# Performance work log

Hardware: AMD Instinct MI355X
Metric: run time of the kernel (lower is better)

## Reference

```python
import jax, jax.numpy as jnp
import numpy as np

Z = 10        # number of negative samples per item
LAMB = 0.01   # L2 regularization weight


def setup_inputs() -> dict:
    key = jax.random.key(0)
    k = jax.random.split(key, 7)
    WE, DE, V, D, B, NG = 300, 256, 50000, 100000, 4096, 10
    return {
        "rv": jax.random.normal(k[0], (WE, V), dtype=jnp.float32),      # word embedding table (frozen in original)
        "rd": jax.random.normal(k[1], (DE, D), dtype=jnp.float32),      # document embedding table
        "proj": jax.random.normal(k[2], (DE, WE), dtype=jnp.float32) * (1.0 / np.sqrt(WE)),
        "beta": jax.random.uniform(k[3], (DE,), dtype=jnp.float32),
        "word_ids": jax.random.randint(k[4], (B, NG), 0, V),
        "doc_ids": jax.random.randint(k[5], (B,), 0, D),
        "neg_ids": jax.random.randint(k[6], (B, Z), 0, D),
    }


def reference(rv, rd, proj, beta, word_ids, doc_ids, neg_ids):
    # g: mean of n-gram word embeddings per sample -> (we, B)
    g = rv[:, word_ids].mean(axis=2)
    # norm: per-sample L2 normalization
    normed = g / jnp.linalg.norm(g, axis=0, keepdims=True)
    # f: project into document space -> (de, B)
    t_pre = proj @ normed
    # standardize across the batch (torch .std is unbiased, ddof=1);
    # NOTE: original divides by sqrt(std), faithfully reproduced
    mean = t_pre.mean(axis=1, keepdims=True)
    std = jnp.std(t_pre, axis=1, ddof=1, keepdims=True)
    t = jnp.clip((t_pre - mean) / jnp.sqrt(std) + beta[:, None], -1.0, 1.0)  # hardtanh
    # positive documents: (de, B)
    doc_emb = rd[:, doc_ids]
    p_pos = jnp.clip(jax.nn.sigmoid(jnp.sum(t * doc_emb, axis=0)), -0.999, 0.999)
    log_p = Z * jnp.log(p_pos)  # (B,)
    # negative samples: (de, B, Z)
    neg_emb = rd[:, neg_ids]
    p_neg = jnp.clip(jax.nn.sigmoid(jnp.einsum('db,dbz->bz', t, neg_emb)), -0.999, 0.999)
    nsample_log = jnp.sum(jnp.log(jnp.clip(1.0 - p_neg, 0.01, None)), axis=1)  # (B,)
    log_p_wave = (Z + 1) / (2 * Z) * (log_p + nsample_log)
    B = log_p_wave.shape[0]
    loss = jnp.sum(log_p_wave) / B + LAMB / (2 * B) * (jnp.sum(rd * rd) + jnp.sum(proj * proj))
    return loss
```

## Files before the change

kernel.cpp:

```cpp
#include <hip/hip_runtime.h>
#include <math.h>

#define WE 300
#define DEp 256
#define VV 50000
#define DDim 100000
#define BB 4096
#define NGc 10
#define RVT_STRIDE 304

__device__ __forceinline__ float wave_reduce(float v) {
    #pragma unroll
    for (int o = 32; o > 0; o >>= 1) v += __shfl_down(v, o, 64);
    return v;
}

__device__ __forceinline__ float wave_allreduce(float v) {
    #pragma unroll
    for (int o = 32; o > 0; o >>= 1) v += __shfl_xor(v, o, 64);
    return v;
}

__device__ __forceinline__ float logsigf(float x) {
    return (x >= 0.f) ? -log1pf(expf(-x)) : x - log1pf(expf(x));
}

__global__ void k_init(double* p, int n) {
    int i = blockIdx.x * blockDim.x + threadIdx.x;
    if (i < n) p[i] = 0.0;
}

__global__ __launch_bounds__(256) void k_trd(const float* __restrict__ in,
                                             float* __restrict__ out,
                                             double* __restrict__ reg_acc) {
    __shared__ float4 tile[32 * 64];
    const int N = DDim;
    int n0 = blockIdx.x * 32;
    int t = threadIdx.x;
    float ss = 0.f;
    #pragma unroll
    for (int i = 0; i < 2; ++i) {
        int flat = i * 256 + t;
        int qn = flat & 7;
        int qm = flat >> 3;
        int n = n0 + qn * 4;
        const float* p = in + (size_t)(qm * 4) * N + n;
        float4 v0 = *(const float4*)(p);
        float4 v1 = *(const float4*)(p + N);
        float4 v2 = *(const float4*)(p + 2 * (size_t)N);
        float4 v3 = *(const float4*)(p + 3 * (size_t)N);
        ss += v0.x * v0.x + v0.y * v0.y + v0.z * v0.z + v0.w * v0.w;
        ss += v1.x * v1.x + v1.y * v1.y + v1.z * v1.z + v1.w * v1.w;
        ss += v2.x * v2.x + v2.y * v2.y + v2.z * v2.z + v2.w * v2.w;
        ss += v3.x * v3.x + v3.y * v3.y + v3.z * v3.z + v3.w * v3.w;
        int r0 = qn * 4;
        tile[(r0 + 0) * 64 + (qm ^ (r0 + 0))] = make_float4(v0.x, v1.x, v2.x, v3.x);
        tile[(r0 + 1) * 64 + (qm ^ (r0 + 1))] = make_float4(v0.y, v1.y, v2.y, v3.y);
        tile[(r0 + 2) * 64 + (qm ^ (r0 + 2))] = make_float4(v0.z, v1.z, v2.z, v3.z);
        tile[(r0 + 3) * 64 + (qm ^ (r0 + 3))] = make_float4(v0.w, v1.w, v2.w, v3.w);
    }
    __syncthreads();
    size_t base = (size_t)n0 * DEp;
    #pragma unroll
    for (int i = 0; i < 8; ++i) {
        int j = i * 256 + t;
        int nl = j >> 6;
        int m4 = j & 63;
        *(float4*)(out + base + (size_t)j * 4) = tile[nl * 64 + (m4 ^ nl)];
    }
    float r = wave_reduce(ss);
    __shared__ float part[4];
    int lane = t & 63, wv = t >> 6;
    if (lane == 0) part[wv] = r;
    __syncthreads();
    if (t == 0)
        atomicAdd(reg_acc, (double)(part[0] + part[1] + part[2] + part[3]));
}

__global__ __launch_bounds__(256) void k_trv(const float* __restrict__ in,
                                             float* __restrict__ out) {
    __shared__ float4 tile[32 * 80];
    const int N = VV;
    int n0 = blockIdx.x * 32;
    int t = threadIdx.x;
    #pragma unroll
    for (int i = 0; i < 3; ++i) {
        int flat = i * 256 + t;
        if (flat < 600) {
            int qn = flat & 7;
            int qm = flat >> 3;
            int n = n0 + qn * 4;
            float4 v0, v1, v2, v3;
            if (n < N) {
                const float* p = in + (size_t)(qm * 4) * N + n;
                v0 = *(const float4*)(p);
                v1 = *(const float4*)(p + N);
                v2 = *(const float4*)(p + 2 * (size_t)N);
                v3 = *(const float4*)(p + 3 * (size_t)N);
            } else {
                v0 = v1 = v2 = v3 = make_float4(0.f, 0.f, 0.f, 0.f);
            }
            int r0 = qn * 4;
            tile[(r0 + 0) * 80 + (qm ^ ((r0 + 0) & 7))] = make_float4(v0.x, v1.x, v2.x, v3.x);
            tile[(r0 + 1) * 80 + (qm ^ ((r0 + 1) & 7))] = make_float4(v0.y, v1.y, v2.y, v3.y);
            tile[(r0 + 2) * 80 + (qm ^ ((r0 + 2) & 7))] = make_float4(v0.z, v1.z, v2.z, v3.z);
            tile[(r0 + 3) * 80 + (qm ^ ((r0 + 3) & 7))] = make_float4(v0.w, v1.w, v2.w, v3.w);
        }
    }
    __syncthreads();
    size_t base = (size_t)n0 * (RVT_STRIDE / 4);
    float4* out4 = (float4*)out;
    for (int i = 0; i < 10; ++i) {
        int j = i * 256 + t;
        if (j < 2432) {
            int nl = j / 76;
            int m4 = j - nl * 76;
            if (n0 + nl < N)
                out4[base + j] = tile[nl * 80 + (m4 ^ (nl & 7))];
        }
    }
}


__global__ __launch_bounds__(256) void k_gather2(const float* __restrict__ rvT,
                                                 const int* __restrict__ wid,
                                                 float* __restrict__ normed) {
    int wv = threadIdx.x >> 6, lane = threadIdx.x & 63;
    int b = blockIdx.x * 4 + wv;
    int id = 0;
    if (lane < NGc) id = wid[b * NGc + lane];
    float4 a  = make_float4(0.f, 0.f, 0.f, 0.f);
    float4 a2 = make_float4(0.f, 0.f, 0.f, 0.f);
    #pragma unroll
    for (int ng = 0; ng < NGc; ++ng) {
        int rid = __shfl(id, ng, 64);
        const float* row = rvT + (size_t)rid * RVT_STRIDE;
        float4 v = *(const float4*)(row + lane * 4);
        a.x += v.x; a.y += v.y; a.z += v.z; a.w += v.w;
        if (lane < 11) {
            float4 w = *(const float4*)(row + 256 + lane * 4);
            a2.x += w.x; a2.y += w.y; a2.z += w.z; a2.w += w.w;
        }
    }
    a.x *= 0.1f; a.y *= 0.1f; a.z *= 0.1f; a.w *= 0.1f;
    a2.x *= 0.1f; a2.y *= 0.1f; a2.z *= 0.1f; a2.w *= 0.1f;
    float ss = a.x * a.x + a.y * a.y + a.z * a.z + a.w * a.w
             + a2.x * a2.x + a2.y * a2.y + a2.z * a2.z + a2.w * a2.w;
    float s = wave_allreduce(ss);
    float s_inv = 1.0f / sqrtf(s);
    float* orow = normed + (size_t)b * WE;
    *(float4*)(orow + lane * 4) =
        make_float4(a.x * s_inv, a.y * s_inv, a.z * s_inv, a.w * s_inv);
    if (lane < 11)
        *(float4*)(orow + 256 + lane * 4) =
            make_float4(a2.x * s_inv, a2.y * s_inv, a2.z * s_inv, a2.w * s_inv);
}

__global__ __launch_bounds__(256) void k_loss2(const float* __restrict__ tpre,
                                               const float* __restrict__ meanf,
                                               const float* __restrict__ scalef,
                                               const float* __restrict__ beta,
                                               const float* __restrict__ rdT,
                                               const int* __restrict__ doc_ids,
                                               const int* __restrict__ neg_ids,
                                               double* __restrict__ acc) {
    int wv = threadIdx.x >> 6, lane = threadIdx.x & 63;
    int b = blockIdx.x * 4 + wv;

    float4 t4  = *(const float4*)(tpre + (size_t)b * DEp + lane * 4);
    float4 m4  = *(const float4*)(meanf + lane * 4);
    float4 sc4 = *(const float4*)(scalef + lane * 4);
    float4 be4 = *(const float4*)(beta + lane * 4);
    float tv0 = fminf(1.f, fmaxf(-1.f, (t4.x - m4.x) * sc4.x + be4.x));
    float tv1 = fminf(1.f, fmaxf(-1.f, (t4.y - m4.y) * sc4.y + be4.y));
    float tv2 = fminf(1.f, fmaxf(-1.f, (t4.z - m4.z) * sc4.z + be4.z));
    float tv3 = fminf(1.f, fmaxf(-1.f, (t4.w - m4.w) * sc4.w + be4.w));

    int id = 0;
    if (lane == 0) id = doc_ids[b];
    else if (lane < 11) id = neg_ids[b * NGc + lane - 1];

    float xv = 0.f;
    #pragma unroll
    for (int j = 0; j < 11; ++j) {
        int rid = __shfl(id, j, 64);
        float4 r4 = *(const float4*)(rdT + (size_t)rid * DEp + lane * 4);
        float p = tv0 * r4.x + tv1 * r4.y + tv2 * r4.z + tv3 * r4.w;
        p = wave_allreduce(p);
        if (lane == j) xv = p;
    }
    float contrib = 0.f;
    if (lane == 0)      contrib = 10.f * fminf(logsigf(xv), -1.0005003e-3f);
    else if (lane < 11) contrib = fmaxf(logsigf(-xv), -4.6051702f);
    #pragma unroll
    for (int o = 8; o > 0; o >>= 1) contrib += __shfl_down(contrib, o, 16);

    __shared__ float bp[4];
    if (lane == 0) bp[wv] = contrib;
    __syncthreads();
    if (threadIdx.x == 0)
        atomicAdd(acc, (double)(0.55f * (bp[0] + bp[1] + bp[2] + bp[3])));
}


__global__ __launch_bounds__(320) void k_gather(const float* __restrict__ rv,
                                                const int* __restrict__ wid,
                                                float* __restrict__ normed) {
    int b = blockIdx.x;
    int tid = threadIdx.x;
    __shared__ int ids[NGc];
    __shared__ float wpart[5];
    __shared__ float s_inv;
    if (tid < NGc) ids[tid] = wid[b * NGc + tid];
    __syncthreads();
    float g = 0.f;
    if (tid < WE) {
        const float* row = rv + (size_t)tid * VV;
        #pragma unroll
        for (int ng = 0; ng < NGc; ++ng) g += row[ids[ng]];
        g *= 0.1f;
    }
    float r = wave_reduce(g * g);
    int lane = tid & 63, wv = tid >> 6;
    if (lane == 0) wpart[wv] = r;
    __syncthreads();
    if (tid == 0) {
        float s = wpart[0] + wpart[1] + wpart[2] + wpart[3] + wpart[4];
        s_inv = 1.0f / sqrtf(s);
    }
    __syncthreads();
    if (tid < WE) normed[(size_t)b * WE + tid] = g * s_inv;
}

__global__ __launch_bounds__(256) void k_loss(const float* __restrict__ tpre,
                                              const float* __restrict__ meanf,
                                              const float* __restrict__ scalef,
                                              const float* __restrict__ beta,
                                              const float* __restrict__ rd,
                                              const int* __restrict__ doc_ids,
                                              const int* __restrict__ neg_ids,
                                              double* __restrict__ acc) {
    int b = blockIdx.x;
    int de = threadIdx.x;
    float t = tpre[(size_t)b * DEp + de];
    float tv = (t - meanf[de]) * scalef[de] + beta[de];
    tv = fminf(1.f, fmaxf(-1.f, tv));
    const float* rdrow = rd + (size_t)de * DDim;
    __shared__ int ids[11];
    if (de == 0) ids[0] = doc_ids[b];
    if (de >= 1 && de < 11) ids[de] = neg_ids[b * NGc + de - 1];
    __syncthreads();
    float prod[11];
    #pragma unroll
    for (int j = 0; j < 11; ++j) prod[j] = tv * rdrow[ids[j]];
    __shared__ float part[11][4];
    int lane = de & 63, wv = de >> 6;
    #pragma unroll
    for (int j = 0; j < 11; ++j) {
        float r = wave_reduce(prod[j]);
        if (lane == 0) part[j][wv] = r;
    }
    __syncthreads();
    if (de == 0) {
        float x0 = part[0][0] + part[0][1] + part[0][2] + part[0][3];
        float total = 10.f * fminf(logsigf(x0), -1.0005003e-3f);
        #pragma unroll
        for (int j = 1; j < 11; ++j) {
            float xj = part[j][0] + part[j][1] + part[j][2] + part[j][3];
            total += fmaxf(logsigf(-xj), -4.6051702f);
        }
        atomicAdd(acc, (double)(0.55f * total));
    }
}


__global__ __launch_bounds__(256) void k_gemm(const float* __restrict__ proj,
                                              const float* __restrict__ normed,
                                              float* __restrict__ tpre) {
    __shared__ float As[64 * 33];
    __shared__ float Bs[64 * 33];
    int tid = threadIdx.x;
    int tx = tid & 15, ty = tid >> 4;
    int de0 = blockIdx.y * 64;
    int b0  = blockIdx.x * 64;
    float acc[4][4] = {};
    int f = tid & 7, r0 = tid >> 3;
    for (int kt = 0; kt < 10; ++kt) {
        int k0 = kt * 32;
        __syncthreads();
        for (int rr = r0; rr < 64; rr += 32) {
            int k = k0 + f * 4;
            float4 va = make_float4(0.f, 0.f, 0.f, 0.f);
            float4 vb = make_float4(0.f, 0.f, 0.f, 0.f);
            if (k + 3 < WE) {
                va = *(const float4*)(proj + (size_t)(de0 + rr) * WE + k);
                vb = *(const float4*)(normed + (size_t)(b0 + rr) * WE + k);
            }
            float* ap = &As[rr * 33 + f * 4];
            ap[0] = va.x; ap[1] = va.y; ap[2] = va.z; ap[3] = va.w;
            float* bp = &Bs[rr * 33 + f * 4];
            bp[0] = vb.x; bp[1] = vb.y; bp[2] = vb.z; bp[3] = vb.w;
        }
        __syncthreads();
        #pragma unroll
        for (int k = 0; k < 32; ++k) {
            float a[4], bv[4];
            #pragma unroll
            for (int i = 0; i < 4; ++i) a[i] = As[(tx * 4 + i) * 33 + k];
            #pragma unroll
            for (int j = 0; j < 4; ++j) bv[j] = Bs[(ty * 4 + j) * 33 + k];
            #pragma unroll
            for (int j = 0; j < 4; ++j)
                #pragma unroll
                for (int i = 0; i < 4; ++i) acc[j][i] += a[i] * bv[j];
        }
    }
    #pragma unroll
    for (int jb = 0; jb < 4; ++jb) {
        int b = b0 + ty * 4 + jb;
        float4 v = make_float4(acc[jb][0], acc[jb][1], acc[jb][2], acc[jb][3]);
        *(float4*)(tpre + (size_t)b * DEp + de0 + tx * 4) = v;
    }
}

__global__ __launch_bounds__(256) void k_stats1(const float* __restrict__ tpre,
                                                double* __restrict__ rowsum,
                                                double* __restrict__ rowsq) {
    int de = threadIdx.x;
    int c0 = blockIdx.x * 64;
    float s = 0.f, ss = 0.f;
    for (int i = 0; i < 64; ++i) {
        float v = tpre[(size_t)(c0 + i) * DEp + de];
        s += v; ss += v * v;
    }
    atomicAdd(&rowsum[de], (double)s);
    atomicAdd(&rowsq[de], (double)ss);
}

__global__ void k_stats2(const double* __restrict__ rowsum, const double* __restrict__ rowsq,
                         float* __restrict__ meanf, float* __restrict__ scalef) {
    int de = threadIdx.x;
    double s = rowsum[de], ss = rowsq[de];
    double mean = s / (double)BB;
    double var = (ss - s * s / (double)BB) / (double)(BB - 1);
    double stdv = sqrt(var);
    meanf[de]  = (float)mean;
    scalef[de] = (float)(1.0 / sqrt(stdv));
}

__global__ __launch_bounds__(256) void k_reg(const float4* __restrict__ p, int n4,
                                             double* __restrict__ acc) {
    int idx = blockIdx.x * blockDim.x + threadIdx.x;
    int stride = gridDim.x * blockDim.x;
    float s = 0.f;
    for (int i = idx; i < n4; i += stride) {
        float4 v = p[i];
        s += v.x * v.x + v.y * v.y + v.z * v.z + v.w * v.w;
    }
    float r = wave_reduce(s);
    __shared__ float part[4];
    int lane = threadIdx.x & 63, wv = threadIdx.x >> 6;
    if (lane == 0) part[wv] = r;
    __syncthreads();
    if (threadIdx.x == 0)
        atomicAdd(acc, (double)(part[0] + part[1] + part[2] + part[3]));
}

__global__ void k_final(const double* __restrict__ accs, float* __restrict__ out) {
    double loss = accs[0] / (double)BB + (0.01 / (2.0 * (double)BB)) * (accs[1] + accs[2]);
    out[0] = (float)loss;
}

extern "C" void kernel_launch(void* const* d_in, const int* in_sizes, int n_in,
                              void* d_out, int out_size, void* d_ws, size_t ws_size,
                              hipStream_t stream) {
    const float* rv   = (const float*)d_in[0];
    const float* rd   = (const float*)d_in[1];
    const float* proj = (const float*)d_in[2];
    const float* beta = (const float*)d_in[3];
    const int* wid    = (const int*)d_in[4];
    const int* doc    = (const int*)d_in[5];
    const int* neg    = (const int*)d_in[6];
    float* out = (float*)d_out;
    char* ws = (char*)d_ws;

    const size_t off_big    = 0;
    const size_t off_normed = 102400000;
    const size_t off_tpre   = off_normed + 4915200;
    const size_t off_small  = off_tpre + 4194304;
    const size_t need = off_small + 1024 + 1024 + 2048 + 2048 + 24;

    if (ws_size >= need) {
        float*  rvT    = (float*)(ws + off_big);
        float*  rdT    = (float*)(ws + off_big);
        float*  normed = (float*)(ws + off_normed);
        float*  tpre   = (float*)(ws + off_tpre);
        float*  meanf  = (float*)(ws + off_small);
        float*  scalef = (float*)(ws + off_small + 1024);
        double* rowsum = (double*)(ws + off_small + 2048);
        double* rowsq  = (double*)(ws + off_small + 4096);
        double* accs   = (double*)(ws + off_small + 6144);

        k_init<<<3, 256, 0, stream>>>(rowsum, 515);
        k_trv<<<1563, 256, 0, stream>>>(rv, rvT);
        k_gather2<<<BB / 4, 256, 0, stream>>>(rvT, wid, normed);
        k_gemm<<<dim3(64, 4), 256, 0, stream>>>(proj, normed, tpre);
        k_stats1<<<64, 256, 0, stream>>>(tpre, rowsum, rowsq);
        k_stats2<<<1, 256, 0, stream>>>(rowsum, rowsq, meanf, scalef);
        k_trd<<<3125, 256, 0, stream>>>(rd, rdT, accs + 1);
        k_loss2<<<BB / 4, 256, 0, stream>>>(tpre, meanf, scalef, beta, rdT, doc, neg, accs);
        k_reg<<<75, 256, 0, stream>>>((const float4*)proj, 19200, accs + 2);
        k_final<<<1, 1, 0, stream>>>(accs, out);
    } else {
        float*  normed = (float*)(ws);
        float*  tpre   = (float*)(ws + 4915200);
        float*  meanf  = (float*)(ws + 9109504);
        float*  scalef = (float*)(ws + 9110528);
        double* rowsum = (double*)(ws + 9111552);
        double* rowsq  = (double*)(ws + 9113600);
        double* accs   = (double*)(ws + 9115648);

        k_init<<<3, 256, 0, stream>>>(rowsum, 515);
        k_gather<<<BB, 320, 0, stream>>>(rv, wid, normed);
        k_gemm<<<dim3(64, 4), 256, 0, stream>>>(proj, normed, tpre);
        k_stats1<<<64, 256, 0, stream>>>(tpre, rowsum, rowsq);
        k_stats2<<<1, 256, 0, stream>>>(rowsum, rowsq, meanf, scalef);
        k_loss<<<BB, 256, 0, stream>>>(tpre, meanf, scalef, beta, rd, doc, neg, accs);
        k_reg<<<1024, 256, 0, stream>>>((const float4*)rd, 6400000, accs + 1);
        k_reg<<<75, 256, 0, stream>>>((const float4*)proj, 19200, accs + 2);
        k_final<<<1, 1, 0, stream>>>(accs, out);
    }
}
```

Before: 295.7 us.

## Make transpose kernels persistent with register prefetch of next tile

Converts the rd and rv transpose kernels into grid-stride persistent loops launched with 1024 blocks. Each block loads the next 32-column tile into registers while it writes the current tile from shared memory, so global loads overlap with stores. This cuts block launch overhead and hides load latency, in exchange for more registers per thread and fewer blocks in flight.

```diff
diff --git a/kernel.cpp b/kernel.cpp
--- a/kernel.cpp
+++ b/kernel.cpp
@@ -34,42 +34,66 @@
                                              float* __restrict__ out,
                                              double* __restrict__ reg_acc) {
     __shared__ float4 tile[32 * 64];
+    __shared__ float part[4];
     const int N = DDim;
-    int n0 = blockIdx.x * 32;
+    const int NT = 3125;
     int t = threadIdx.x;
+    int qn = t & 7;
+    int qmA = t >> 3;
+    int qmB = qmA + 32;
+    int G = gridDim.x;
     float ss = 0.f;
-    #pragma unroll
-    for (int i = 0; i < 2; ++i) {
-        int flat = i * 256 + t;
-        int qn = flat & 7;
-        int qm = flat >> 3;
-        int n = n0 + qn * 4;
-        const float* p = in + (size_t)(qm * 4) * N + n;
-        float4 v0 = *(const float4*)(p);
-        float4 v1 = *(const float4*)(p + N);
-        float4 v2 = *(const float4*)(p + 2 * (size_t)N);
-        float4 v3 = *(const float4*)(p + 3 * (size_t)N);
-        ss += v0.x * v0.x + v0.y * v0.y + v0.z * v0.z + v0.w * v0.w;
-        ss += v1.x * v1.x + v1.y * v1.y + v1.z * v1.z + v1.w * v1.w;
-        ss += v2.x * v2.x + v2.y * v2.y + v2.z * v2.z + v2.w * v2.w;
-        ss += v3.x * v3.x + v3.y * v3.y + v3.z * v3.z + v3.w * v3.w;
-        int r0 = qn * 4;
-        tile[(r0 + 0) * 64 + (qm ^ (r0 + 0))] = make_float4(v0.x, v1.x, v2.x, v3.x);
-        tile[(r0 + 1) * 64 + (qm ^ (r0 + 1))] = make_float4(v0.y, v1.y, v2.y, v3.y);
-        tile[(r0 + 2) * 64 + (qm ^ (r0 + 2))] = make_float4(v0.z, v1.z, v2.z, v3.z);
-        tile[(r0 + 3) * 64 + (qm ^ (r0 + 3))] = make_float4(v0.w, v1.w, v2.w, v3.w);
-    }
-    __syncthreads();
-    size_t base = (size_t)n0 * DEp;
-    #pragma unroll
-    for (int i = 0; i < 8; ++i) {
-        int j = i * 256 + t;
-        int nl = j >> 6;
-        int m4 = j & 63;
-        *(float4*)(out + base + (size_t)j * 4) = tile[nl * 64 + (m4 ^ nl)];
+    float4 rA[4], rB[4];
+    int cur = blockIdx.x;
+    {
+        int n = cur * 32 + qn * 4;
+        const float* pA = in + (size_t)(qmA * 4) * N + n;
+        const float* pB = in + (size_t)(qmB * 4) * N + n;
+        #pragma unroll
+        for (int e = 0; e < 4; ++e) rA[e] = *(const float4*)(pA + (size_t)e * N);
+        #pragma unroll
+        for (int e = 0; e < 4; ++e) rB[e] = *(const float4*)(pB + (size_t)e * N);
+    }
+    while (true) {
+        int nxt = cur + G;
+        __syncthreads();
+        #pragma unroll
+        for (int e = 0; e < 4; ++e) {
+            ss += rA[e].x * rA[e].x + rA[e].y * rA[e].y + rA[e].z * rA[e].z + rA[e].w * rA[e].w;
+            ss += rB[e].x * rB[e].x + rB[e].y * rB[e].y + rB[e].z * rB[e].z + rB[e].w * rB[e].w;
+        }
+        int c0 = qn * 4;
+        tile[(c0 + 0) * 64 + (qmA ^ (c0 + 0))] = make_float4(rA[0].x, rA[1].x, rA[2].x, rA[3].x);
+        tile[(c0 + 1) * 64 + (qmA ^ (c0 + 1))] = make_float4(rA[0].y, rA[1].y, rA[2].y, rA[3].y);
+        tile[(c0 + 2) * 64 + (qmA ^ (c0 + 2))] = make_float4(rA[0].z, rA[1].z, rA[2].z, rA[3].z);
+        tile[(c0 + 3) * 64 + (qmA ^ (c0 + 3))] = make_float4(rA[0].w, rA[1].w, rA[2].w, rA[3].w);
+        tile[(c0 + 0) * 64 + (qmB ^ (c0 + 0))] = make_float4(rB[0].x, rB[1].x, rB[2].x, rB[3].x);
+        tile[(c0 + 1) * 64 + (qmB ^ (c0 + 1))] = make_float4(rB[0].y, rB[1].y, rB[2].y, rB[3].y);
+        tile[(c0 + 2) * 64 + (qmB ^ (c0 + 2))] = make_float4(rB[0].z, rB[1].z, rB[2].z, rB[3].z);
+        tile[(c0 + 3) * 64 + (qmB ^ (c0 + 3))] = make_float4(rB[0].w, rB[1].w, rB[2].w, rB[3].w);
+        __syncthreads();
+        bool more = (nxt < NT);
+        if (more) {
+            int n = nxt * 32 + qn * 4;
+            const float* pA = in + (size_t)(qmA * 4) * N + n;
+            const float* pB = in + (size_t)(qmB * 4) * N + n;
+            #pragma unroll
+            for (int e = 0; e < 4; ++e) rA[e] = *(const float4*)(pA + (size_t)e * N);
+            #pragma unroll
+            for (int e = 0; e < 4; ++e) rB[e] = *(const float4*)(pB + (size_t)e * N);
+        }
+        size_t base = (size_t)cur * (32 * DEp);
+        #pragma unroll
+        for (int i = 0; i < 8; ++i) {
+            int j = i * 256 + t;
+            int nl = j >> 6;
+            int m4 = j & 63;
+            *(float4*)(out + base + (size_t)j * 4) = tile[nl * 64 + (m4 ^ nl)];
+        }
+        if (!more) break;
+        cur = nxt;
     }
     float r = wave_reduce(ss);
-    __shared__ float part[4];
     int lane = t & 63, wv = t >> 6;
     if (lane == 0) part[wv] = r;
     __syncthreads();
@@ -81,43 +105,76 @@
                                              float* __restrict__ out) {
     __shared__ float4 tile[32 * 80];
     const int N = VV;
-    int n0 = blockIdx.x * 32;
+    const int NT = 1563;
     int t = threadIdx.x;
-    #pragma unroll
-    for (int i = 0; i < 3; ++i) {
-        int flat = i * 256 + t;
-        if (flat < 600) {
-            int qn = flat & 7;
-            int qm = flat >> 3;
-            int n = n0 + qn * 4;
-            float4 v0, v1, v2, v3;
-            if (n < N) {
-                const float* p = in + (size_t)(qm * 4) * N + n;
-                v0 = *(const float4*)(p);
-                v1 = *(const float4*)(p + N);
-                v2 = *(const float4*)(p + 2 * (size_t)N);
-                v3 = *(const float4*)(p + 3 * (size_t)N);
-            } else {
-                v0 = v1 = v2 = v3 = make_float4(0.f, 0.f, 0.f, 0.f);
+    int qn = t & 7;
+    int qmA = t >> 3;
+    int qmB = qmA + 32;
+    int qmC = qmA + 64;
+    bool hasC = (t < 88);
+    int G = gridDim.x;
+    float4 rA[4], rB[4], rC[4];
+    int cur = blockIdx.x;
+    {
+        int n = cur * 32 + qn * 4;
+        bool ok = (n < N);
+        const float* pA = in + (size_t)(qmA * 4) * N + n;
+        const float* pB = in + (size_t)(qmB * 4) * N + n;
+        const float* pC = in + (size_t)(qmC * 4) * N + n;
+        #pragma unroll
+        for (int e = 0; e < 4; ++e) {
+            rA[e] = ok ? *(const float4*)(pA + (size_t)e * N) : make_float4(0.f, 0.f, 0.f, 0.f);
+            rB[e] = ok ? *(const float4*)(pB + (size_t)e * N) : make_float4(0.f, 0.f, 0.f, 0.f);
+            rC[e] = (ok && hasC) ? *(const float4*)(pC + (size_t)e * N) : make_float4(0.f, 0.f, 0.f, 0.f);
+        }
+    }
+    while (true) {
+        int nxt = cur + G;
+        __syncthreads();
+        int c0 = qn * 4;
+        tile[(c0 + 0) * 80 + (qmA ^ ((c0 + 0) & 7))] = make_float4(rA[0].x, rA[1].x, rA[2].x, rA[3].x);
+        tile[(c0 + 1) * 80 + (qmA ^ ((c0 + 1) & 7))] = make_float4(rA[0].y, rA[1].y, rA[2].y, rA[3].y);
+        tile[(c0 + 2) * 80 + (qmA ^ ((c0 + 2) & 7))] = make_float4(rA[0].z, rA[1].z, rA[2].z, rA[3].z);
+        tile[(c0 + 3) * 80 + (qmA ^ ((c0 + 3) & 7))] = make_float4(rA[0].w, rA[1].w, rA[2].w, rA[3].w);
+        tile[(c0 + 0) * 80 + (qmB ^ ((c0 + 0) & 7))] = make_float4(rB[0].x, rB[1].x, rB[2].x, rB[3].x);
+        tile[(c0 + 1) * 80 + (qmB ^ ((c0 + 1) & 7))] = make_float4(rB[0].y, rB[1].y, rB[2].y, rB[3].y);
+        tile[(c0 + 2) * 80 + (qmB ^ ((c0 + 2) & 7))] = make_float4(rB[0].z, rB[1].z, rB[2].z, rB[3].z);
+        tile[(c0 + 3) * 80 + (qmB ^ ((c0 + 3) & 7))] = make_float4(rB[0].w, rB[1].w, rB[2].w, rB[3].w);
+        if (hasC) {
+            tile[(c0 + 0) * 80 + (qmC ^ ((c0 + 0) & 7))] = make_float4(rC[0].x, rC[1].x, rC[2].x, rC[3].x);
+            tile[(c0 + 1) * 80 + (qmC ^ ((c0 + 1) & 7))] = make_float4(rC[0].y, rC[1].y, rC[2].y, rC[3].y);
+            tile[(c0 + 2) * 80 + (qmC ^ ((c0 + 2) & 7))] = make_float4(rC[0].z, rC[1].z, rC[2].z, rC[3].z);
+            tile[(c0 + 3) * 80 + (qmC ^ ((c0 + 3) & 7))] = make_float4(rC[0].w, rC[1].w, rC[2].w, rC[3].w);
+        }
+        __syncthreads();
+        bool more = (nxt < NT);
+        if (more) {
+            int n = nxt * 32 + qn * 4;
+            bool ok = (n < N);
+            const float* pA = in + (size_t)(qmA * 4) * N + n;
+            const float* pB = in + (size_t)(qmB * 4) * N + n;
+            const float* pC = in + (size_t)(qmC * 4) * N + n;
+            #pragma unroll
+            for (int e = 0; e < 4; ++e) {
+                rA[e] = ok ? *(const float4*)(pA + (size_t)e * N) : make_float4(0.f, 0.f, 0.f, 0.f);
+                rB[e] = ok ? *(const float4*)(pB + (size_t)e * N) : make_float4(0.f, 0.f, 0.f, 0.f);
+                rC[e] = (ok && hasC) ? *(const float4*)(pC + (size_t)e * N) : make_float4(0.f, 0.f, 0.f, 0.f);
             }
-            int r0 = qn * 4;
-            tile[(r0 + 0) * 80 + (qm ^ ((r0 + 0) & 7))] = make_float4(v0.x, v1.x, v2.x, v3.x);
-            tile[(r0 + 1) * 80 + (qm ^ ((r0 + 1) & 7))] = make_float4(v0.y, v1.y, v2.y, v3.y);
-            tile[(r0 + 2) * 80 + (qm ^ ((r0 + 2) & 7))] = make_float4(v0.z, v1.z, v2.z, v3.z);
-            tile[(r0 + 3) * 80 + (qm ^ ((r0 + 3) & 7))] = make_float4(v0.w, v1.w, v2.w, v3.w);
-        }
-    }
-    __syncthreads();
-    size_t base = (size_t)n0 * (RVT_STRIDE / 4);
-    float4* out4 = (float4*)out;
-    for (int i = 0; i < 10; ++i) {
-        int j = i * 256 + t;
-        if (j < 2432) {
-            int nl = j / 76;
-            int m4 = j - nl * 76;
-            if (n0 + nl < N)
-                out4[base + j] = tile[nl * 80 + (m4 ^ (nl & 7))];
-        }
+        }
+        size_t base = (size_t)cur * (32 * 76);
+        float4* out4 = (float4*)out;
+        #pragma unroll
+        for (int i = 0; i < 10; ++i) {
+            int j = i * 256 + t;
+            if (j < 2432) {
+                int nl = j / 76;
+                int m4 = j - nl * 76;
+                if (cur * 32 + nl < N)
+                    out4[base + j] = tile[nl * 80 + (m4 ^ (nl & 7))];
+            }
+        }
+        if (!more) break;
+        cur = nxt;
     }
 }
 
@@ -402,12 +459,12 @@
         double* accs   = (double*)(ws + off_small + 6144);
 
         k_init<<<3, 256, 0, stream>>>(rowsum, 515);
-        k_trv<<<1563, 256, 0, stream>>>(rv, rvT);
+        k_trv<<<1024, 256, 0, stream>>>(rv, rvT);
         k_gather2<<<BB / 4, 256, 0, stream>>>(rvT, wid, normed);
         k_gemm<<<dim3(64, 4), 256, 0, stream>>>(proj, normed, tpre);
         k_stats1<<<64, 256, 0, stream>>>(tpre, rowsum, rowsq);
         k_stats2<<<1, 256, 0, stream>>>(rowsum, rowsq, meanf, scalef);
-        k_trd<<<3125, 256, 0, stream>>>(rd, rdT, accs + 1);
+        k_trd<<<1024, 256, 0, stream>>>(rd, rdT, accs + 1);
         k_loss2<<<BB / 4, 256, 0, stream>>>(tpre, meanf, scalef, beta, rdT, doc, neg, accs);
         k_reg<<<75, 256, 0, stream>>>((const float4*)proj, 19200, accs + 2);
         k_final<<<1, 1, 0, stream>>>(accs, out);
```

Result: no change. 299.3 us (+1.2%).

## Drop embedding table transposes and gather columns directly from original layout

Applied to the files above, without the earlier changes.

Removes the kernels that transposed the word and document embedding tables into workspace, and gathers the needed columns straight from the original column-major layout with strided scalar loads. The document-table regularization sum moves back into a separate reduction kernel. This avoids writing and rereading full transposed copies of both large tables, but each gathered element is now an uncoalesced scattered load that wastes most of each fetched sector.

```diff
diff --git a/kernel.cpp b/kernel.cpp
--- a/kernel.cpp
+++ b/kernel.cpp
@@ -7,7 +7,6 @@
 #define DDim 100000
 #define BB 4096
 #define NGc 10
-#define RVT_STRIDE 304
 
 __device__ __forceinline__ float wave_reduce(float v) {
     #pragma unroll
@@ -30,137 +29,45 @@
     if (i < n) p[i] = 0.0;
 }
 
-__global__ __launch_bounds__(256) void k_trd(const float* __restrict__ in,
-                                             float* __restrict__ out,
-                                             double* __restrict__ reg_acc) {
-    __shared__ float4 tile[32 * 64];
-    const int N = DDim;
-    int n0 = blockIdx.x * 32;
-    int t = threadIdx.x;
-    float ss = 0.f;
-    #pragma unroll
-    for (int i = 0; i < 2; ++i) {
-        int flat = i * 256 + t;
-        int qn = flat & 7;
-        int qm = flat >> 3;
-        int n = n0 + qn * 4;
-        const float* p = in + (size_t)(qm * 4) * N + n;
-        float4 v0 = *(const float4*)(p);
-        float4 v1 = *(const float4*)(p + N);
-        float4 v2 = *(const float4*)(p + 2 * (size_t)N);
-        float4 v3 = *(const float4*)(p + 3 * (size_t)N);
-        ss += v0.x * v0.x + v0.y * v0.y + v0.z * v0.z + v0.w * v0.w;
-        ss += v1.x * v1.x + v1.y * v1.y + v1.z * v1.z + v1.w * v1.w;
-        ss += v2.x * v2.x + v2.y * v2.y + v2.z * v2.z + v2.w * v2.w;
-        ss += v3.x * v3.x + v3.y * v3.y + v3.z * v3.z + v3.w * v3.w;
-        int r0 = qn * 4;
-        tile[(r0 + 0) * 64 + (qm ^ (r0 + 0))] = make_float4(v0.x, v1.x, v2.x, v3.x);
-        tile[(r0 + 1) * 64 + (qm ^ (r0 + 1))] = make_float4(v0.y, v1.y, v2.y, v3.y);
-        tile[(r0 + 2) * 64 + (qm ^ (r0 + 2))] = make_float4(v0.z, v1.z, v2.z, v3.z);
-        tile[(r0 + 3) * 64 + (qm ^ (r0 + 3))] = make_float4(v0.w, v1.w, v2.w, v3.w);
-    }
-    __syncthreads();
-    size_t base = (size_t)n0 * DEp;
-    #pragma unroll
-    for (int i = 0; i < 8; ++i) {
-        int j = i * 256 + t;
-        int nl = j >> 6;
-        int m4 = j & 63;
-        *(float4*)(out + base + (size_t)j * 4) = tile[nl * 64 + (m4 ^ nl)];
-    }
-    float r = wave_reduce(ss);
-    __shared__ float part[4];
-    int lane = t & 63, wv = t >> 6;
-    if (lane == 0) part[wv] = r;
-    __syncthreads();
-    if (t == 0)
-        atomicAdd(reg_acc, (double)(part[0] + part[1] + part[2] + part[3]));
-}
-
-__global__ __launch_bounds__(256) void k_trv(const float* __restrict__ in,
-                                             float* __restrict__ out) {
-    __shared__ float4 tile[32 * 80];
-    const int N = VV;
-    int n0 = blockIdx.x * 32;
-    int t = threadIdx.x;
-    #pragma unroll
-    for (int i = 0; i < 3; ++i) {
-        int flat = i * 256 + t;
-        if (flat < 600) {
-            int qn = flat & 7;
-            int qm = flat >> 3;
-            int n = n0 + qn * 4;
-            float4 v0, v1, v2, v3;
-            if (n < N) {
-                const float* p = in + (size_t)(qm * 4) * N + n;
-                v0 = *(const float4*)(p);
-                v1 = *(const float4*)(p + N);
-                v2 = *(const float4*)(p + 2 * (size_t)N);
-                v3 = *(const float4*)(p + 3 * (size_t)N);
-            } else {
-                v0 = v1 = v2 = v3 = make_float4(0.f, 0.f, 0.f, 0.f);
-            }
-            int r0 = qn * 4;
-            tile[(r0 + 0) * 80 + (qm ^ ((r0 + 0) & 7))] = make_float4(v0.x, v1.x, v2.x, v3.x);
-            tile[(r0 + 1) * 80 + (qm ^ ((r0 + 1) & 7))] = make_float4(v0.y, v1.y, v2.y, v3.y);
-            tile[(r0 + 2) * 80 + (qm ^ ((r0 + 2) & 7))] = make_float4(v0.z, v1.z, v2.z, v3.z);
-            tile[(r0 + 3) * 80 + (qm ^ ((r0 + 3) & 7))] = make_float4(v0.w, v1.w, v2.w, v3.w);
-        }
-    }
-    __syncthreads();
-    size_t base = (size_t)n0 * (RVT_STRIDE / 4);
-    float4* out4 = (float4*)out;
-    for (int i = 0; i < 10; ++i) {
-        int j = i * 256 + t;
-        if (j < 2432) {
-            int nl = j / 76;
-            int m4 = j - nl * 76;
-            if (n0 + nl < N)
-                out4[base + j] = tile[nl * 80 + (m4 ^ (nl & 7))];
-        }
-    }
-}
-
-
-__global__ __launch_bounds__(256) void k_gather2(const float* __restrict__ rvT,
-                                                 const int* __restrict__ wid,
-                                                 float* __restrict__ normed) {
+__global__ __launch_bounds__(256) void k_gather2d(const float* __restrict__ rv,
+                                                  const int* __restrict__ wid,
+                                                  float* __restrict__ normed) {
     int wv = threadIdx.x >> 6, lane = threadIdx.x & 63;
     int b = blockIdx.x * 4 + wv;
     int id = 0;
     if (lane < NGc) id = wid[b * NGc + lane];
-    float4 a  = make_float4(0.f, 0.f, 0.f, 0.f);
-    float4 a2 = make_float4(0.f, 0.f, 0.f, 0.f);
+    float a[4]  = {0.f, 0.f, 0.f, 0.f};
+    float a2[4] = {0.f, 0.f, 0.f, 0.f};
     #pragma unroll
     for (int ng = 0; ng < NGc; ++ng) {
         int rid = __shfl(id, ng, 64);
-        const float* row = rvT + (size_t)rid * RVT_STRIDE;
-        float4 v = *(const float4*)(row + lane * 4);
-        a.x += v.x; a.y += v.y; a.z += v.z; a.w += v.w;
+        const float* col = rv + rid;
+        #pragma unroll
+        for (int e = 0; e < 4; ++e) a[e] += col[(size_t)(4 * lane + e) * VV];
         if (lane < 11) {
-            float4 w = *(const float4*)(row + 256 + lane * 4);
-            a2.x += w.x; a2.y += w.y; a2.z += w.z; a2.w += w.w;
+            #pragma unroll
+            for (int e = 0; e < 4; ++e) a2[e] += col[(size_t)(256 + 4 * lane + e) * VV];
         }
     }
-    a.x *= 0.1f; a.y *= 0.1f; a.z *= 0.1f; a.w *= 0.1f;
-    a2.x *= 0.1f; a2.y *= 0.1f; a2.z *= 0.1f; a2.w *= 0.1f;
-    float ss = a.x * a.x + a.y * a.y + a.z * a.z + a.w * a.w
-             + a2.x * a2.x + a2.y * a2.y + a2.z * a2.z + a2.w * a2.w;
+    #pragma unroll
+    for (int e = 0; e < 4; ++e) { a[e] *= 0.1f; a2[e] *= 0.1f; }
+    float ss = a[0] * a[0] + a[1] * a[1] + a[2] * a[2] + a[3] * a[3]
+             + a2[0] * a2[0] + a2[1] * a2[1] + a2[2] * a2[2] + a2[3] * a2[3];
     float s = wave_allreduce(ss);
     float s_inv = 1.0f / sqrtf(s);
     float* orow = normed + (size_t)b * WE;
     *(float4*)(orow + lane * 4) =
-        make_float4(a.x * s_inv, a.y * s_inv, a.z * s_inv, a.w * s_inv);
+        make_float4(a[0] * s_inv, a[1] * s_inv, a[2] * s_inv, a[3] * s_inv);
     if (lane < 11)
         *(float4*)(orow + 256 + lane * 4) =
-            make_float4(a2.x * s_inv, a2.y * s_inv, a2.z * s_inv, a2.w * s_inv);
-}
-
-__global__ __launch_bounds__(256) void k_loss2(const float* __restrict__ tpre,
+            make_float4(a2[0] * s_inv, a2[1] * s_inv, a2[2] * s_inv, a2[3] * s_inv);
+}
+
+__global__ __launch_bounds__(256) void k_lossd(const float* __restrict__ tpre,
                                                const float* __restrict__ meanf,
                                                const float* __restrict__ scalef,
                                                const float* __restrict__ beta,
-                                               const float* __restrict__ rdT,
+                                               const float* __restrict__ rd,
                                                const int* __restrict__ doc_ids,
                                                const int* __restrict__ neg_ids,
                                                double* __restrict__ acc) {
@@ -184,8 +91,11 @@
     #pragma unroll
     for (int j = 0; j < 11; ++j) {
         int rid = __shfl(id, j, 64);
-        float4 r4 = *(const float4*)(rdT + (size_t)rid * DEp + lane * 4);
-        float p = tv0 * r4.x + tv1 * r4.y + tv2 * r4.z + tv3 * r4.w;
+        const float* col = rd + rid;
+        float p = tv0 * col[(size_t)(4 * lane + 0) * DDim]
+                + tv1 * col[(size_t)(4 * lane + 1) * DDim]
+                + tv2 * col[(size_t)(4 * lane + 2) * DDim]
+                + tv3 * col[(size_t)(4 * lane + 3) * DDim];
         p = wave_allreduce(p);
         if (lane == j) xv = p;
     }
@@ -200,77 +110,6 @@
     __syncthreads();
     if (threadIdx.x == 0)
         atomicAdd(acc, (double)(0.55f * (bp[0] + bp[1] + bp[2] + bp[3])));
-}
-
-
-__global__ __launch_bounds__(320) void k_gather(const float* __restrict__ rv,
-                                                const int* __restrict__ wid,
-                                                float* __restrict__ normed) {
-    int b = blockIdx.x;
-    int tid = threadIdx.x;
-    __shared__ int ids[NGc];
-    __shared__ float wpart[5];
-    __shared__ float s_inv;
-    if (tid < NGc) ids[tid] = wid[b * NGc + tid];
-    __syncthreads();
-    float g = 0.f;
-    if (tid < WE) {
-        const float* row = rv + (size_t)tid * VV;
-        #pragma unroll
-        for (int ng = 0; ng < NGc; ++ng) g += row[ids[ng]];
-        g *= 0.1f;
-    }
-    float r = wave_reduce(g * g);
-    int lane = tid & 63, wv = tid >> 6;
-    if (lane == 0) wpart[wv] = r;
-    __syncthreads();
-    if (tid == 0) {
-        float s = wpart[0] + wpart[1] + wpart[2] + wpart[3] + wpart[4];
-        s_inv = 1.0f / sqrtf(s);
-    }
-    __syncthreads();
-    if (tid < WE) normed[(size_t)b * WE + tid] = g * s_inv;
-}
-
-__global__ __launch_bounds__(256) void k_loss(const float* __restrict__ tpre,
-                                              const float* __restrict__ meanf,
-                                              const float* __restrict__ scalef,
-                                              const float* __restrict__ beta,
-                                              const float* __restrict__ rd,
-                                              const int* __restrict__ doc_ids,
-                                              const int* __restrict__ neg_ids,
-                                              double* __restrict__ acc) {
-    int b = blockIdx.x;
-    int de = threadIdx.x;
-    float t = tpre[(size_t)b * DEp + de];
-    float tv = (t - meanf[de]) * scalef[de] + beta[de];
-    tv = fminf(1.f, fmaxf(-1.f, tv));
-    const float* rdrow = rd + (size_t)de * DDim;
-    __shared__ int ids[11];
-    if (de == 0) ids[0] = doc_ids[b];
-    if (de >= 1 && de < 11) ids[de] = neg_ids[b * NGc + de - 1];
-    __syncthreads();
-    float prod[11];
-    #pragma unroll
-    for (int j = 0; j < 11; ++j) prod[j] = tv * rdrow[ids[j]];
-    __shared__ float part[11][4];
-    int lane = de & 63, wv = de >> 6;
-    #pragma unroll
-    for (int j = 0; j < 11; ++j) {
-        float r = wave_reduce(prod[j]);
-        if (lane == 0) part[j][wv] = r;
-    }
-    __syncthreads();
-    if (de == 0) {
-        float x0 = part[0][0] + part[0][1] + part[0][2] + part[0][3];
-        float total = 10.f * fminf(logsigf(x0), -1.0005003e-3f);
-        #pragma unroll
-        for (int j = 1; j < 11; ++j) {
-            float xj = part[j][0] + part[j][1] + part[j][2] + part[j][3];
-            total += fmaxf(logsigf(-xj), -4.6051702f);
-        }
-        atomicAdd(acc, (double)(0.55f * total));
-    }
 }
 
 
@@ -384,50 +223,21 @@
     float* out = (float*)d_out;
     char* ws = (char*)d_ws;
 
-    const size_t off_big    = 0;
-    const size_t off_normed = 102400000;
-    const size_t off_tpre   = off_normed + 4915200;
-    const size_t off_small  = off_tpre + 4194304;
-    const size_t need = off_small + 1024 + 1024 + 2048 + 2048 + 24;
-
-    if (ws_size >= need) {
-        float*  rvT    = (float*)(ws + off_big);
-        float*  rdT    = (float*)(ws + off_big);
-        float*  normed = (float*)(ws + off_normed);
-        float*  tpre   = (float*)(ws + off_tpre);
-        float*  meanf  = (float*)(ws + off_small);
-        float*  scalef = (float*)(ws + off_small + 1024);
-        double* rowsum = (double*)(ws + off_small + 2048);
-        double* rowsq  = (double*)(ws + off_small + 4096);
-        double* accs   = (double*)(ws + off_small + 6144);
-
-        k_init<<<3, 256, 0, stream>>>(rowsum, 515);
-        k_trv<<<1563, 256, 0, stream>>>(rv, rvT);
-        k_gather2<<<BB / 4, 256, 0, stream>>>(rvT, wid, normed);
-        k_gemm<<<dim3(64, 4), 256, 0, stream>>>(proj, normed, tpre);
-        k_stats1<<<64, 256, 0, stream>>>(tpre, rowsum, rowsq);
-        k_stats2<<<1, 256, 0, stream>>>(rowsum, rowsq, meanf, scalef);
-        k_trd<<<3125, 256, 0, stream>>>(rd, rdT, accs + 1);
-        k_loss2<<<BB / 4, 256, 0, stream>>>(tpre, meanf, scalef, beta, rdT, doc, neg, accs);
-        k_reg<<<75, 256, 0, stream>>>((const float4*)proj, 19200, accs + 2);
-        k_final<<<1, 1, 0, stream>>>(accs, out);
-    } else {
-        float*  normed = (float*)(ws);
-        float*  tpre   = (float*)(ws + 4915200);
-        float*  meanf  = (float*)(ws + 9109504);
-        float*  scalef = (float*)(ws + 9110528);
-        double* rowsum = (double*)(ws + 9111552);
-        double* rowsq  = (double*)(ws + 9113600);
-        double* accs   = (double*)(ws + 9115648);
-
-        k_init<<<3, 256, 0, stream>>>(rowsum, 515);
-        k_gather<<<BB, 320, 0, stream>>>(rv, wid, normed);
-        k_gemm<<<dim3(64, 4), 256, 0, stream>>>(proj, normed, tpre);
-        k_stats1<<<64, 256, 0, stream>>>(tpre, rowsum, rowsq);
-        k_stats2<<<1, 256, 0, stream>>>(rowsum, rowsq, meanf, scalef);
-        k_loss<<<BB, 256, 0, stream>>>(tpre, meanf, scalef, beta, rd, doc, neg, accs);
-        k_reg<<<1024, 256, 0, stream>>>((const float4*)rd, 6400000, accs + 1);
-        k_reg<<<75, 256, 0, stream>>>((const float4*)proj, 19200, accs + 2);
-        k_final<<<1, 1, 0, stream>>>(accs, out);
-    }
-}
+    float*  normed = (float*)(ws);
+    float*  tpre   = (float*)(ws + 4915200);
+    float*  meanf  = (float*)(ws + 9109504);
+    float*  scalef = (float*)(ws + 9110528);
+    double* rowsum = (double*)(ws + 9111552);
+    double* rowsq  = (double*)(ws + 9113600);
+    double* accs   = (double*)(ws + 9115648);
+
+    k_init<<<3, 256, 0, stream>>>(rowsum, 515);
+    k_gather2d<<<BB / 4, 256, 0, stream>>>(rv, wid, normed);
+    k_gemm<<<dim3(64, 4), 256, 0, stream>>>(proj, normed, tpre);
+    k_stats1<<<64, 256, 0, stream>>>(tpre, rowsum, rowsq);
+    k_stats2<<<1, 256, 0, stream>>>(rowsum, rowsq, meanf, scalef);
+    k_lossd<<<BB / 4, 256, 0, stream>>>(tpre, meanf, scalef, beta, rd, doc, neg, accs);
+    k_reg<<<1024, 256, 0, stream>>>((const float4*)rd, 6400000, accs + 1);
+    k_reg<<<75, 256, 0, stream>>>((const float4*)proj, 19200, accs + 2);
+    k_final<<<1, 1, 0, stream>>>(accs, out);
+}
```

New measurement: 638.9 us. 116% more time.

## Write only referenced columns in transposes via bitmaps; fuse batch stats into GEMM

Applied to the files above, without the earlier changes.

Adds a kernel that builds bitmaps of the word and document ids referenced in this batch. The rv and rd transpose kernels then write back only the referenced columns, while still reading the full tables, which k_trd needs for the L2 sum anyway. It also folds the per-row sum and sum-of-squares statistics into the GEMM epilogue through shared-memory and then global atomics, which removes the separate k_stats1 pass. The cost is an extra marking kernel with global atomics, plus float atomics in shared memory, which may slightly change the summation order.

```diff
diff --git a/kernel.cpp b/kernel.cpp
--- a/kernel.cpp
+++ b/kernel.cpp
@@ -25,18 +25,38 @@
     return (x >= 0.f) ? -log1pf(expf(-x)) : x - log1pf(expf(x));
 }
 
-__global__ void k_init(double* p, int n) {
+__global__ void k_init(unsigned* p, int n) {
     int i = blockIdx.x * blockDim.x + threadIdx.x;
-    if (i < n) p[i] = 0.0;
+    if (i < n) p[i] = 0u;
+}
+
+__global__ __launch_bounds__(256) void k_mark(const int* __restrict__ wid,
+                                              const int* __restrict__ doc,
+                                              const int* __restrict__ neg,
+                                              unsigned* __restrict__ bmv,
+                                              unsigned* __restrict__ bmd) {
+    int i = blockIdx.x * 256 + threadIdx.x;
+    if (i < BB * NGc) {
+        int id = wid[i];
+        atomicOr(&bmv[id >> 5], 1u << (id & 31));
+    } else if (i < BB * NGc + BB) {
+        int id = doc[i - BB * NGc];
+        atomicOr(&bmd[id >> 5], 1u << (id & 31));
+    } else if (i < BB * NGc + BB + BB * NGc) {
+        int id = neg[i - BB * NGc - BB];
+        atomicOr(&bmd[id >> 5], 1u << (id & 31));
+    }
 }
 
 __global__ __launch_bounds__(256) void k_trd(const float* __restrict__ in,
                                              float* __restrict__ out,
-                                             double* __restrict__ reg_acc) {
+                                             double* __restrict__ reg_acc,
+                                             const unsigned* __restrict__ bmd) {
     __shared__ float4 tile[32 * 64];
     const int N = DDim;
     int n0 = blockIdx.x * 32;
     int t = threadIdx.x;
+    unsigned ref = bmd[blockIdx.x];
     float ss = 0.f;
     #pragma unroll
     for (int i = 0; i < 2; ++i) {
@@ -66,7 +86,8 @@
         int j = i * 256 + t;
         int nl = j >> 6;
         int m4 = j & 63;
-        *(float4*)(out + base + (size_t)j * 4) = tile[nl * 64 + (m4 ^ nl)];
+        if ((ref >> nl) & 1)
+            *(float4*)(out + base + (size_t)j * 4) = tile[nl * 64 + (m4 ^ nl)];
     }
     float r = wave_reduce(ss);
     __shared__ float part[4];
@@ -78,11 +99,13 @@
 }
 
 __global__ __launch_bounds__(256) void k_trv(const float* __restrict__ in,
-                                             float* __restrict__ out) {
+                                             float* __restrict__ out,
+                                             const unsigned* __restrict__ bmv) {
     __shared__ float4 tile[32 * 80];
     const int N = VV;
     int n0 = blockIdx.x * 32;
     int t = threadIdx.x;
+    unsigned ref = bmv[blockIdx.x];
     #pragma unroll
     for (int i = 0; i < 3; ++i) {
         int flat = i * 256 + t;
@@ -115,7 +138,7 @@
         if (j < 2432) {
             int nl = j / 76;
             int m4 = j - nl * 76;
-            if (n0 + nl < N)
+            if (((ref >> nl) & 1) && (n0 + nl < N))
                 out4[base + j] = tile[nl * 80 + (m4 ^ (nl & 7))];
         }
     }
@@ -276,9 +299,13 @@
 
 __global__ __launch_bounds__(256) void k_gemm(const float* __restrict__ proj,
                                               const float* __restrict__ normed,
-                                              float* __restrict__ tpre) {
+                                              float* __restrict__ tpre,
+                                              double* __restrict__ rowsum,
+                                              double* __restrict__ rowsq) {
     __shared__ float As[64 * 33];
     __shared__ float Bs[64 * 33];
+    __shared__ float sSum[64];
+    __shared__ float sSq[64];
     int tid = threadIdx.x;
     int tx = tid & 15, ty = tid >> 4;
     int de0 = blockIdx.y * 64;
@@ -321,20 +348,24 @@
         float4 v = make_float4(acc[jb][0], acc[jb][1], acc[jb][2], acc[jb][3]);
         *(float4*)(tpre + (size_t)b * DEp + de0 + tx * 4) = v;
     }
-}
-
-__global__ __launch_bounds__(256) void k_stats1(const float* __restrict__ tpre,
-                                                double* __restrict__ rowsum,
-                                                double* __restrict__ rowsq) {
-    int de = threadIdx.x;
-    int c0 = blockIdx.x * 64;
-    float s = 0.f, ss = 0.f;
-    for (int i = 0; i < 64; ++i) {
-        float v = tpre[(size_t)(c0 + i) * DEp + de];
-        s += v; ss += v * v;
-    }
-    atomicAdd(&rowsum[de], (double)s);
-    atomicAdd(&rowsq[de], (double)ss);
+    if (tid < 64) { sSum[tid] = 0.f; sSq[tid] = 0.f; }
+    __syncthreads();
+    #pragma unroll
+    for (int i = 0; i < 4; ++i) {
+        float ls = 0.f, lq = 0.f;
+        #pragma unroll
+        for (int jb = 0; jb < 4; ++jb) {
+            float v = acc[jb][i];
+            ls += v; lq += v * v;
+        }
+        atomicAdd(&sSum[tx * 4 + i], ls);
+        atomicAdd(&sSq[tx * 4 + i], lq);
+    }
+    __syncthreads();
+    if (tid < 64) {
+        atomicAdd(&rowsum[de0 + tid], (double)sSum[tid]);
+        atomicAdd(&rowsq[de0 + tid], (double)sSq[tid]);
+    }
 }
 
 __global__ void k_stats2(const double* __restrict__ rowsum, const double* __restrict__ rowsq,
@@ -388,26 +419,28 @@
     const size_t off_normed = 102400000;
     const size_t off_tpre   = off_normed + 4915200;
     const size_t off_small  = off_tpre + 4194304;
-    const size_t need = off_small + 1024 + 1024 + 2048 + 2048 + 24;
+    const size_t need = off_small + 2048 + 2048 + 2048 + 64 + 6272 + 12500;
 
     if (ws_size >= need) {
-        float*  rvT    = (float*)(ws + off_big);
-        float*  rdT    = (float*)(ws + off_big);
-        float*  normed = (float*)(ws + off_normed);
-        float*  tpre   = (float*)(ws + off_tpre);
-        float*  meanf  = (float*)(ws + off_small);
-        float*  scalef = (float*)(ws + off_small + 1024);
-        double* rowsum = (double*)(ws + off_small + 2048);
-        double* rowsq  = (double*)(ws + off_small + 4096);
-        double* accs   = (double*)(ws + off_small + 6144);
-
-        k_init<<<3, 256, 0, stream>>>(rowsum, 515);
-        k_trv<<<1563, 256, 0, stream>>>(rv, rvT);
+        float*    rvT    = (float*)(ws + off_big);
+        float*    rdT    = (float*)(ws + off_big);
+        float*    normed = (float*)(ws + off_normed);
+        float*    tpre   = (float*)(ws + off_tpre);
+        float*    meanf  = (float*)(ws + off_small);
+        float*    scalef = (float*)(ws + off_small + 1024);
+        double*   rowsum = (double*)(ws + off_small + 2048);
+        double*   rowsq  = (double*)(ws + off_small + 4096);
+        double*   accs   = (double*)(ws + off_small + 6144);
+        unsigned* bmv    = (unsigned*)(ws + off_small + 6208);
+        unsigned* bmd    = (unsigned*)(ws + off_small + 6208 + 6272);
+
+        k_init<<<23, 256, 0, stream>>>((unsigned*)(ws + off_small + 2048), 5733);
+        k_mark<<<336, 256, 0, stream>>>(wid, doc, neg, bmv, bmd);
+        k_trv<<<1563, 256, 0, stream>>>(rv, rvT, bmv);
         k_gather2<<<BB / 4, 256, 0, stream>>>(rvT, wid, normed);
-        k_gemm<<<dim3(64, 4), 256, 0, stream>>>(proj, normed, tpre);
-        k_stats1<<<64, 256, 0, stream>>>(tpre, rowsum, rowsq);
+        k_gemm<<<dim3(64, 4), 256, 0, stream>>>(proj, normed, tpre, rowsum, rowsq);
         k_stats2<<<1, 256, 0, stream>>>(rowsum, rowsq, meanf, scalef);
-        k_trd<<<3125, 256, 0, stream>>>(rd, rdT, accs + 1);
+        k_trd<<<3125, 256, 0, stream>>>(rd, rdT, accs + 1, bmd);
         k_loss2<<<BB / 4, 256, 0, stream>>>(tpre, meanf, scalef, beta, rdT, doc, neg, accs);
         k_reg<<<75, 256, 0, stream>>>((const float4*)proj, 19200, accs + 2);
         k_final<<<1, 1, 0, stream>>>(accs, out);
@@ -420,10 +453,9 @@
         double* rowsq  = (double*)(ws + 9113600);
         double* accs   = (double*)(ws + 9115648);
 
-        k_init<<<3, 256, 0, stream>>>(rowsum, 515);
+        k_init<<<5, 256, 0, stream>>>((unsigned*)(ws + 9111552), 1030);
         k_gather<<<BB, 320, 0, stream>>>(rv, wid, normed);
-        k_gemm<<<dim3(64, 4), 256, 0, stream>>>(proj, normed, tpre);
-        k_stats1<<<64, 256, 0, stream>>>(tpre, rowsum, rowsq);
+        k_gemm<<<dim3(64, 4), 256, 0, stream>>>(proj, normed, tpre, rowsum, rowsq);
         k_stats2<<<1, 256, 0, stream>>>(rowsum, rowsq, meanf, scalef);
         k_loss<<<BB, 256, 0, stream>>>(tpre, meanf, scalef, beta, rd, doc, neg, accs);
         k_reg<<<1024, 256, 0, stream>>>((const float4*)rd, 6400000, accs + 1);
```

Result: no change. 299.7 us (+1.3%).
